# Optimization experiments

Hardware: AMD Instinct MI355X
Metric: run time of the kernel (lower is better)

Reference implementation:

```python
import jax, jax.numpy as jnp
import numpy as np

H = 16          # num_heads
KVH = 4         # num_kv_heads
HD = 128        # head_dim = dim // num_heads
BASE = 10000.0  # rope_base
EPS = 1.1920928955078125e-07  # torch F.rms_norm default eps = finfo(fp32).eps


def rotate_half(x):
    h = x.shape[-1] // 2
    return jnp.concatenate([-x[..., h:], x[..., :h]], axis=-1)


def rms_norm(x):
    return x * jax.lax.rsqrt(jnp.mean(x * x, axis=-1, keepdims=True) + EPS)


def setup_inputs() -> dict:
    key = jax.random.key(0)
    ks = jax.random.split(key, 5)
    D = H * HD
    KVD = KVH * HD
    s = 0.02
    x = jax.random.normal(ks[0], (4, 2048, D), jnp.float32)
    Wq = jax.random.normal(ks[1], (D, D), jnp.float32) * s
    Wk = jax.random.normal(ks[2], (KVD, D), jnp.float32) * s
    Wv = jax.random.normal(ks[3], (KVD, D), jnp.float32) * s
    Wproj = jax.random.normal(ks[4], (D, D), jnp.float32) * s
    q_gain = jnp.full((H,), 1.0, jnp.float32)
    return {"x": x, "Wq": Wq, "Wk": Wk, "Wv": Wv, "Wproj": Wproj, "q_gain": q_gain}


def reference(x, Wq, Wk, Wv, Wproj, q_gain):
    B, T, D = x.shape
    # QKV projections (bias-free), reshape to [B, heads, T, head_dim]
    q = (x @ Wq.T).reshape(B, T, H, HD).transpose(0, 2, 1, 3)
    k = (x @ Wk.T).reshape(B, T, KVH, HD).transpose(0, 2, 1, 3)
    v = (x @ Wv.T).reshape(B, T, KVH, HD).transpose(0, 2, 1, 3)
    # QK RMSNorm (no learned weight)
    q = rms_norm(q)
    k = rms_norm(k)
    # Rotary embedding tables [T, HD]
    t = jnp.arange(T, dtype=jnp.float32)
    inv_freq = 1.0 / (BASE ** (jnp.arange(0, HD, 2, dtype=jnp.float32) / HD))
    freqs = jnp.outer(t, inv_freq)
    emb = jnp.concatenate([freqs, freqs], axis=-1)
    cos, sin = jnp.cos(emb), jnp.sin(emb)
    # RoPE + per-head gain on q
    q = (q * cos + rotate_half(q) * sin) * q_gain[None, :, None, None]
    k = k * cos + rotate_half(k) * sin
    # GQA: repeat_interleave kv heads to match q heads
    groups = H // KVH
    k = jnp.repeat(k, groups, axis=1)
    v = jnp.repeat(v, groups, axis=1)
    # Causal scaled dot-product attention
    scores = jnp.einsum('bhqd,bhkd->bhqk', q, k) / np.float32(np.sqrt(HD))
    mask = jnp.tril(jnp.ones((T, T), dtype=bool))
    scores = jnp.where(mask, scores, -jnp.inf)
    attn = jax.nn.softmax(scores, axis=-1)
    y = jnp.einsum('bhqk,bhkd->bhqd', attn, v)
    y = y.transpose(0, 2, 1, 3).reshape(B, T, D)
    return y @ Wproj.T
```

## Files before the change

### kernel.cpp

```cpp
#include <hip/hip_runtime.h>
#include <math.h>


typedef float f32x4 __attribute__((ext_vector_type(4)));
typedef __bf16 bf16x8 __attribute__((ext_vector_type(8)));
typedef __bf16 bf16x4 __attribute__((ext_vector_type(4)));

__device__ __forceinline__ void load_lds16(const __bf16* g, __bf16* l) {
    __builtin_amdgcn_global_load_lds(
        (const __attribute__((address_space(1))) void*)g,
        (__attribute__((address_space(3))) void*)l, 16, 0, 0);
}

__global__ __launch_bounds__(256) void cvt_f32_bf16(
    const float* __restrict__ src, __bf16* __restrict__ dst, int n)
{
    int i = (blockIdx.x * 256 + threadIdx.x) * 4;
    if (i < n) {
        float4 v = *(const float4*)(src + i);
        bf16x4 o = {(__bf16)v.x, (__bf16)v.y, (__bf16)v.z, (__bf16)v.w};
        *(bf16x4*)(dst + i) = o;
    }
}

template <int NI, typename OutT>
__global__ __launch_bounds__(512, 2) void gemm256(
    const __bf16* __restrict__ A, const __bf16* __restrict__ W,
    OutT* __restrict__ C, int M, int N, int K)
{
    constexpr int BN = 64 * NI;
    const int bn = blockIdx.x, bm = blockIdx.y;
    const int tid = threadIdx.x;
    const int lane = tid & 63;
    const int wave = tid >> 6;
    const int quad = lane >> 4, l16 = lane & 15;
    const int wm2 = wave >> 2;
    const int wn4 = wave & 3;

    __shared__ __bf16 As[2][256 * 64];
    __shared__ __bf16 Bs[2][BN * 64];

    f32x4 acc[8][NI] = {};

    const int sr = tid >> 3;
    const int sc = tid & 7;
    const int scs = sc ^ (sr & 7);

    const __bf16* Ag = A + (size_t)(bm * 256 + sr) * K + scs * 8;
    const __bf16* Wg = W + (size_t)(bn * BN + sr) * K + scs * 8;
    __bf16* Asd = &As[0][0] + sr * 64 + sc * 8;
    __bf16* Bsd = &Bs[0][0] + sr * 64 + sc * 8;

    auto stage = [&](int t, int h) {
        const int k0 = t * 64;
#pragma unroll
        for (int ra = 0; ra < 4; ++ra)
            load_lds16(Ag + (size_t)(ra * 64) * K + k0,
                       Asd + h * 16384 + ra * 4096);
#pragma unroll
        for (int rb = 0; rb < NI; ++rb)
            load_lds16(Wg + (size_t)(rb * 64) * K + k0,
                       Bsd + h * (BN * 64) + rb * 4096);
    };
    auto wait_prev = [&]() {
        if constexpr (NI == 4) asm volatile("s_waitcnt vmcnt(8)" ::: "memory");
        else                   asm volatile("s_waitcnt vmcnt(6)" ::: "memory");
    };

    const int NT = K / 64;

    stage(0, 0);
    stage(1, 1);
    wait_prev();
    asm volatile("" ::: "memory");
    __builtin_amdgcn_s_barrier();
    asm volatile("" ::: "memory");

    for (int t = 0; t < NT; ++t) {
        const int h = t & 1;
        const __bf16* Ab = &As[h][0];
        const __bf16* Bb = &Bs[h][0];

        bf16x8 bfr[NI][2];
#pragma unroll
        for (int ph = 0; ph < 4; ++ph) {
            bf16x8 af[2][2];
#pragma unroll
            for (int j = 0; j < 2; ++j)
#pragma unroll
                for (int ks = 0; ks < 2; ++ks)
                    af[j][ks] = *(const bf16x8*)(
                        Ab + (wm2 * 128 + (ph * 2 + j) * 16 + l16) * 64 +
                        (((ks * 4 + quad) ^ (l16 & 7)) * 8));
            if (ph == 0) {
#pragma unroll
                for (int ni = 0; ni < NI; ++ni)
#pragma unroll
                    for (int ks = 0; ks < 2; ++ks)
                        bfr[ni][ks] = *(const bf16x8*)(
                            Bb + (wn4 * 16 * NI + ni * 16 + l16) * 64 +
                            (((ks * 4 + quad) ^ (l16 & 7)) * 8));
            }
            asm volatile("" ::: "memory");
            __builtin_amdgcn_s_barrier();
            asm volatile("" ::: "memory");
            __builtin_amdgcn_s_setprio(1);
#pragma unroll
            for (int j = 0; j < 2; ++j)
#pragma unroll
                for (int ni = 0; ni < NI; ++ni)
#pragma unroll
                    for (int ks = 0; ks < 2; ++ks)
                        acc[ph * 2 + j][ni] = __builtin_amdgcn_mfma_f32_16x16x32_bf16(
                            af[j][ks], bfr[ni][ks], acc[ph * 2 + j][ni], 0, 0, 0);
            __builtin_amdgcn_s_setprio(0);
            asm volatile("" ::: "memory");
            __builtin_amdgcn_s_barrier();
            asm volatile("" ::: "memory");
        }

        if (t + 2 < NT) {
            stage(t + 2, h);
            wait_prev();
        } else if (t + 1 < NT) {
            asm volatile("s_waitcnt vmcnt(0)" ::: "memory");
        } else {
            break;
        }
        asm volatile("" ::: "memory");
        __builtin_amdgcn_s_barrier();
        asm volatile("" ::: "memory");
    }

#pragma unroll
    for (int mi = 0; mi < 8; ++mi) {
#pragma unroll
        for (int r = 0; r < 4; ++r) {
            int row = bm * 256 + wm2 * 128 + mi * 16 + quad * 4 + r;
            OutT* Cp = C + (size_t)row * N + bn * BN + wn4 * 16 * NI + l16;
#pragma unroll
            for (int ni = 0; ni < NI; ++ni)
                Cp[ni * 16] = (OutT)acc[mi][ni][r];
        }
    }
}

__global__ __launch_bounds__(256) void qk_norm_rope(
    __bf16* __restrict__ q, __bf16* __restrict__ kv,
    const float* __restrict__ q_gain)
{
    const int row = blockIdx.x * 4 + (threadIdx.x >> 6);
    const int lane = threadIdx.x & 63;
    const int BTH = 4 * 2048 * 16;

    __bf16* base;
    int t;
    float gain;
    if (row < BTH) {
        int bt = row >> 4, h = row & 15;
        base = q + (size_t)bt * 2048 + h * 128;
        t = bt & 2047;
        gain = q_gain[h];
    } else {
        int r2 = row - BTH;
        int bt = r2 >> 2, kvh = r2 & 3;
        base = kv + (size_t)bt * 1024 + kvh * 128;
        t = bt & 2047;
        gain = 1.0f;
    }

    float x0 = (float)base[lane];
    float x1 = (float)base[lane + 64];

    float ss = x0 * x0 + x1 * x1;
#pragma unroll
    for (int off = 32; off; off >>= 1) ss += __shfl_xor(ss, off);
    float inv = rsqrtf(ss * (1.0f / 128.0f) + 1.1920928955078125e-07f);
    x0 *= inv; x1 *= inv;

    float freq = exp2f(-(float)lane * 0.20762050593046013f);
    float ang = (float)t * freq;
    float s, c;
    sincosf(ang, &s, &c);
    float o0 = x0 * c - x1 * s;
    float o1 = x1 * c + x0 * s;
    base[lane]      = (__bf16)(o0 * gain);
    base[lane + 64] = (__bf16)(o1 * gain);
}

__global__ __launch_bounds__(256) void transpose_v(
    const __bf16* __restrict__ kv, __bf16* __restrict__ vtout)
{
    __shared__ __bf16 tile[64][65];
    const int b = blockIdx.z;
    const int t0 = blockIdx.x * 64, c0 = blockIdx.y * 64;
    const __bf16* vb = kv + (size_t)b * 2048 * 1024 + 512;
    __bf16* vtb = vtout + (size_t)b * 512 * 2048;
    const int j = threadIdx.x & 63;
    const int r0 = threadIdx.x >> 6;
#pragma unroll
    for (int i = 0; i < 16; ++i) {
        int r = r0 + i * 4;
        tile[r][j] = vb[(size_t)(t0 + r) * 1024 + c0 + j];
    }
    __syncthreads();
#pragma unroll
    for (int i = 0; i < 16; ++i) {
        int r = r0 + i * 4;
        vtb[(size_t)(c0 + r) * 2048 + t0 + j] = tile[j][r];
    }
}

__global__ __launch_bounds__(256, 2) void attn(
    const __bf16* __restrict__ q, const __bf16* __restrict__ kv,
    const __bf16* __restrict__ vt, __bf16* __restrict__ y,
    const float* __restrict__ q_gain)
{
    const int qt = 15 - blockIdx.y;
    const int bh = blockIdx.x;
    const int b = bh >> 4, h = bh & 15, kvh = h >> 2;
    const int tid = threadIdx.x;
    const int wave = tid >> 6, lane = tid & 63;
    const int quad = lane >> 4, l16 = lane & 15;

    __shared__ __bf16 Ks[2][64 * 128];
    __shared__ __bf16 Vts[2][128 * 64];
    __shared__ __bf16 Ps[4 * 16 * 64];

    const int qt0 = qt * 128;
    const int wq = wave * 16;

    bf16x8 qf[2][4];
#pragma unroll
    for (int p = 0; p < 2; ++p) {
        const size_t qrow =
            ((size_t)b * 2048 + qt0 + p * 64 + wq + l16) * 2048 + h * 128;
#pragma unroll
        for (int t = 0; t < 4; ++t)
            qf[p][t] = *(const bf16x8*)(q + qrow + t * 32 + quad * 8);
    }

    f32x4 oacc[2][8] = {};
    float lsum[2][4] = {};

    const float sm_scale = 0.12754635f;
    const float mfix = 11.5f * fabsf(q_gain[h]);

    const size_t kbase = (size_t)b * 2048 * 1024 + kvh * 128;
    const size_t vtbase = (size_t)(b * 4 + kvh) * 128 * 2048;

    const int rowK = lane >> 4, pcK = lane & 15;
    const int rowV = lane >> 3, pcV = lane & 7;

    const int nj = 2 * qt + 2;

    {
#pragma unroll
        for (int r = 0; r < 4; ++r) {
            int rrK = (r * 4 + wave) * 4 + rowK;
            int cK = pcK ^ (rrK & 15);
            load_lds16(kv + kbase + (size_t)rrK * 1024 + cK * 8,
                       &Ks[0][(r * 4 + wave) * 512]);
            int rrV = (r * 4 + wave) * 8 + rowV;
            int cV = pcV ^ (rrV & 7);
            load_lds16(vt + vtbase + (size_t)rrV * 2048 + cV * 8,
                       &Vts[0][(r * 4 + wave) * 512]);
        }
    }

    for (int jt = 0; jt < nj; ++jt) {
        const int cur = jt & 1;

        asm volatile("" ::: "memory");
        __builtin_amdgcn_s_barrier();
        asm volatile("" ::: "memory");

        if (jt + 1 < nj) {
            const int j0n = (jt + 1) * 64;
#pragma unroll
            for (int r = 0; r < 4; ++r) {
                int rrK = (r * 4 + wave) * 4 + rowK;
                int cK = pcK ^ (rrK & 15);
                load_lds16(kv + kbase + (size_t)(j0n + rrK) * 1024 + cK * 8,
                           &Ks[cur ^ 1][(r * 4 + wave) * 512]);
                int rrV = (r * 4 + wave) * 8 + rowV;
                int cV = pcV ^ (rrV & 7);
                load_lds16(vt + vtbase + (size_t)rrV * 2048 + j0n + cV * 8,
                           &Vts[cur ^ 1][(r * 4 + wave) * 512]);
            }
            asm volatile("s_waitcnt vmcnt(8)" ::: "memory");
        } else {
            asm volatile("s_waitcnt vmcnt(0)" ::: "memory");
        }

        asm volatile("" ::: "memory");
        __builtin_amdgcn_s_barrier();
        asm volatile("" ::: "memory");

        const __bf16* Kc = Ks[cur];
        const __bf16* Vc = Vts[cur];

#pragma unroll
        for (int p = 0; p < 2; ++p) {
            const int dlim = 2 * qt + p;
            if (jt > dlim) continue;

            f32x4 sacc[4] = {};
#pragma unroll
            for (int nt = 0; nt < 4; ++nt)
#pragma unroll
                for (int t = 0; t < 4; ++t) {
                    bf16x8 kf = *(const bf16x8*)(
                        Kc + (nt * 16 + l16) * 128 + ((t * 4 + quad) ^ l16) * 8);
                    sacc[nt] = __builtin_amdgcn_mfma_f32_16x16x32_bf16(
                        qf[p][t], kf, sacc[nt], 0, 0, 0);
                }

            if (jt == dlim) {
#pragma unroll
                for (int nt = 0; nt < 4; ++nt) {
                    int kg = nt * 16 + l16;
#pragma unroll
                    for (int r = 0; r < 4; ++r)
                        if (kg > wq + quad * 4 + r) sacc[nt][r] = -3.0e38f;
                }
            }

            float pv4[4][4];
#pragma unroll
            for (int nt = 0; nt < 4; ++nt)
#pragma unroll
                for (int r = 0; r < 4; ++r) {
                    float pv = exp2f((sacc[nt][r] - mfix) * sm_scale);
                    pv4[nt][r] = pv;
                    lsum[p][r] += pv;
                }

            __bf16* Pw = Ps + wave * 1024;
#pragma unroll
            for (int nt = 0; nt < 4; ++nt)
#pragma unroll
                for (int r = 0; r < 4; ++r) {
                    int row = quad * 4 + r;
                    int pc = (nt * 2 + (l16 >> 3)) ^ (row & 7);
                    Pw[row * 64 + pc * 8 + (l16 & 7)] = (__bf16)pv4[nt][r];
                }

#pragma unroll
            for (int kt = 0; kt < 2; ++kt) {
                bf16x8 pf = *(const bf16x8*)(
                    Pw + l16 * 64 + ((kt * 4 + quad) ^ (l16 & 7)) * 8);
#pragma unroll
                for (int vn = 0; vn < 8; ++vn) {
                    bf16x8 vf = *(const bf16x8*)(
                        Vc + (vn * 16 + l16) * 64 + ((kt * 4 + quad) ^ (l16 & 7)) * 8);
                    oacc[p][vn] = __builtin_amdgcn_mfma_f32_16x16x32_bf16(
                        pf, vf, oacc[p][vn], 0, 0, 0);
                }
            }
        }
    }

#pragma unroll
    for (int p = 0; p < 2; ++p) {
#pragma unroll
        for (int r = 0; r < 4; ++r)
#pragma unroll
            for (int off = 8; off; off >>= 1)
                lsum[p][r] += __shfl_xor(lsum[p][r], off);

        const size_t ybase =
            ((size_t)b * 2048 + qt0 + p * 64 + wq) * 2048 + h * 128;
#pragma unroll
        for (int r = 0; r < 4; ++r) {
            float inv = 1.0f / lsum[p][r];
            __bf16* yp = y + ybase + (size_t)(quad * 4 + r) * 2048 + l16;
#pragma unroll
            for (int vn = 0; vn < 8; ++vn)
                yp[vn * 16] = (__bf16)(oacc[p][vn][r] * inv);
        }
    }
}

extern "C" void kernel_launch(void* const* d_in, const int* in_sizes, int n_in,
                              void* d_out, int out_size, void* d_ws, size_t ws_size,
                              hipStream_t stream) {
    const float* x     = (const float*)d_in[0];
    const float* Wq    = (const float*)d_in[1];
    const float* Wk    = (const float*)d_in[2];
    const float* Wv    = (const float*)d_in[3];
    const float* Wproj = (const float*)d_in[4];
    const float* qgain = (const float*)d_in[5];
    float* outp = (float*)d_out;

    __bf16* xb  = (__bf16*)d_ws;
    __bf16* Wqb = xb  + 16777216;
    __bf16* Wkb = Wqb + 4194304;
    __bf16* Wvb = Wkb + 1048576;
    __bf16* Wpb = Wvb + 1048576;
    __bf16* q   = Wpb + 4194304;
    __bf16* kvb = q   + 16777216;
    __bf16* vt  = kvb + 8388608;
    __bf16* y   = q;

    dim3 blk(256);
    cvt_f32_bf16<<<dim3(16777216 / 1024), blk, 0, stream>>>(x, xb, 16777216);
    cvt_f32_bf16<<<dim3(4194304 / 1024), blk, 0, stream>>>(Wq, Wqb, 4194304);
    cvt_f32_bf16<<<dim3(1048576 / 1024), blk, 0, stream>>>(Wk, Wkb, 1048576);
    cvt_f32_bf16<<<dim3(1048576 / 1024), blk, 0, stream>>>(Wv, Wvb, 1048576);
    cvt_f32_bf16<<<dim3(4194304 / 1024), blk, 0, stream>>>(Wproj, Wpb, 4194304);

    gemm256<4, __bf16><<<dim3(8, 32), dim3(512), 0, stream>>>(xb, Wqb, q, 8192, 2048, 2048);
    gemm256<2, __bf16><<<dim3(8, 32), dim3(512), 0, stream>>>(xb, Wkb, kvb, 8192, 1024, 2048);
    qk_norm_rope<<<dim3((4 * 2048 * (16 + 4)) / 4), blk, 0, stream>>>(q, kvb, qgain);
    transpose_v<<<dim3(32, 8, 4), blk, 0, stream>>>(kvb, vt);
    attn<<<dim3(64, 16), blk, 0, stream>>>(q, kvb, vt, y, qgain);
    gemm256<4, float><<<dim3(8, 32), dim3(512), 0, stream>>>(y, Wpb, outp, 8192, 2048, 2048);
}
```

Before: 527.6 us.

## Merge conversion launches and interleave both query halves in attention MFMA loops

The five fp32-to-bf16 conversion launches become one kernel that picks the source array from the flat index. In the attention inner loop, the two 64-row query halves are now processed together: each K and V fragment load feeds two MFMAs, P is staged in two LDS buffers, and MFMA sections run at raised wave priority via s_setprio. This drops the per-half skip, so the second half always computes scores for the extra diagonal tile and relies on masking. It cuts LDS fragment reloads and launch overhead in exchange for more registers and some wasted MFMA work.

Result: faster. 513.1 us (-2.8%).

```diff
diff --git a/kernel.cpp b/kernel.cpp
--- a/kernel.cpp
+++ b/kernel.cpp
@@ -12,15 +12,23 @@
         (__attribute__((address_space(3))) void*)l, 16, 0, 0);
 }
 
-__global__ __launch_bounds__(256) void cvt_f32_bf16(
-    const float* __restrict__ src, __bf16* __restrict__ dst, int n)
+__global__ __launch_bounds__(256) void cvt_all(
+    const float* __restrict__ x,  const float* __restrict__ Wq,
+    const float* __restrict__ Wk, const float* __restrict__ Wv,
+    const float* __restrict__ Wp, __bf16* __restrict__ dst)
 {
-    int i = (blockIdx.x * 256 + threadIdx.x) * 4;
-    if (i < n) {
-        float4 v = *(const float4*)(src + i);
-        bf16x4 o = {(__bf16)v.x, (__bf16)v.y, (__bf16)v.z, (__bf16)v.w};
-        *(bf16x4*)(dst + i) = o;
-    }
+    long long i = ((long long)blockIdx.x * 256 + threadIdx.x) * 4;
+    if (i >= 27262976LL) return;
+    const float* src;
+    long long off;
+    if (i < 16777216LL)      { src = x;  off = i; }
+    else if (i < 20971520LL) { src = Wq; off = i - 16777216LL; }
+    else if (i < 22020096LL) { src = Wk; off = i - 20971520LL; }
+    else if (i < 23068672LL) { src = Wv; off = i - 22020096LL; }
+    else                     { src = Wp; off = i - 23068672LL; }
+    float4 v = *(const float4*)(src + off);
+    bf16x4 o = {(__bf16)v.x, (__bf16)v.y, (__bf16)v.z, (__bf16)v.w};
+    *(bf16x4*)(dst + i) = o;
 }
 
 template <int NI, typename OutT>
@@ -225,7 +233,7 @@
 
     __shared__ __bf16 Ks[2][64 * 128];
     __shared__ __bf16 Vts[2][128 * 64];
-    __shared__ __bf16 Ps[4 * 16 * 64];
+    __shared__ __bf16 Ps[2][4 * 16 * 64];
 
     const int qt0 = qt * 128;
     const int wq = wave * 16;
@@ -300,65 +308,68 @@
         const __bf16* Kc = Ks[cur];
         const __bf16* Vc = Vts[cur];
 
-#pragma unroll
-        for (int p = 0; p < 2; ++p) {
-            const int dlim = 2 * qt + p;
-            if (jt > dlim) continue;
-
-            f32x4 sacc[4] = {};
-#pragma unroll
-            for (int nt = 0; nt < 4; ++nt)
-#pragma unroll
-                for (int t = 0; t < 4; ++t) {
-                    bf16x8 kf = *(const bf16x8*)(
-                        Kc + (nt * 16 + l16) * 128 + ((t * 4 + quad) ^ l16) * 8);
-                    sacc[nt] = __builtin_amdgcn_mfma_f32_16x16x32_bf16(
-                        qf[p][t], kf, sacc[nt], 0, 0, 0);
-                }
-
-            if (jt == dlim) {
+        f32x4 sacc[2][4] = {};
+        __builtin_amdgcn_s_setprio(1);
+#pragma unroll
+        for (int nt = 0; nt < 4; ++nt)
+#pragma unroll
+            for (int t = 0; t < 4; ++t) {
+                bf16x8 kf = *(const bf16x8*)(
+                    Kc + (nt * 16 + l16) * 128 + ((t * 4 + quad) ^ l16) * 8);
+                sacc[0][nt] = __builtin_amdgcn_mfma_f32_16x16x32_bf16(
+                    qf[0][t], kf, sacc[0][nt], 0, 0, 0);
+                sacc[1][nt] = __builtin_amdgcn_mfma_f32_16x16x32_bf16(
+                    qf[1][t], kf, sacc[1][nt], 0, 0, 0);
+            }
+        __builtin_amdgcn_s_setprio(0);
+
+        if (jt >= 2 * qt) {
+            const int dj = (jt - 2 * qt) * 64;
+#pragma unroll
+            for (int p = 0; p < 2; ++p) {
+                const int rel = p * 64 + wq + quad * 4 - dj;
 #pragma unroll
                 for (int nt = 0; nt < 4; ++nt) {
                     int kg = nt * 16 + l16;
 #pragma unroll
                     for (int r = 0; r < 4; ++r)
-                        if (kg > wq + quad * 4 + r) sacc[nt][r] = -3.0e38f;
+                        if (kg > rel + r) sacc[p][nt][r] = -3.0e38f;
                 }
             }
-
-            float pv4[4][4];
+        }
+
+#pragma unroll
+        for (int p = 0; p < 2; ++p) {
+            __bf16* Pw = &Ps[p][0] + wave * 1024;
 #pragma unroll
             for (int nt = 0; nt < 4; ++nt)
 #pragma unroll
                 for (int r = 0; r < 4; ++r) {
-                    float pv = exp2f((sacc[nt][r] - mfix) * sm_scale);
-                    pv4[nt][r] = pv;
+                    float pv = exp2f((sacc[p][nt][r] - mfix) * sm_scale);
                     lsum[p][r] += pv;
-                }
-
-            __bf16* Pw = Ps + wave * 1024;
-#pragma unroll
-            for (int nt = 0; nt < 4; ++nt)
-#pragma unroll
-                for (int r = 0; r < 4; ++r) {
                     int row = quad * 4 + r;
                     int pc = (nt * 2 + (l16 >> 3)) ^ (row & 7);
-                    Pw[row * 64 + pc * 8 + (l16 & 7)] = (__bf16)pv4[nt][r];
+                    Pw[row * 64 + pc * 8 + (l16 & 7)] = (__bf16)pv;
                 }
-
-#pragma unroll
-            for (int kt = 0; kt < 2; ++kt) {
-                bf16x8 pf = *(const bf16x8*)(
-                    Pw + l16 * 64 + ((kt * 4 + quad) ^ (l16 & 7)) * 8);
-#pragma unroll
-                for (int vn = 0; vn < 8; ++vn) {
-                    bf16x8 vf = *(const bf16x8*)(
-                        Vc + (vn * 16 + l16) * 64 + ((kt * 4 + quad) ^ (l16 & 7)) * 8);
-                    oacc[p][vn] = __builtin_amdgcn_mfma_f32_16x16x32_bf16(
-                        pf, vf, oacc[p][vn], 0, 0, 0);
-                }
+        }
+
+        __builtin_amdgcn_s_setprio(1);
+#pragma unroll
+        for (int kt = 0; kt < 2; ++kt) {
+            const int pcc = ((kt * 4 + quad) ^ (l16 & 7)) * 8;
+            bf16x8 pf0 = *(const bf16x8*)(&Ps[0][0] + wave * 1024 + l16 * 64 + pcc);
+            bf16x8 pf1 = *(const bf16x8*)(&Ps[1][0] + wave * 1024 + l16 * 64 + pcc);
+#pragma unroll
+            for (int vn = 0; vn < 8; ++vn) {
+                bf16x8 vf = *(const bf16x8*)(
+                    Vc + (vn * 16 + l16) * 64 + pcc);
+                oacc[0][vn] = __builtin_amdgcn_mfma_f32_16x16x32_bf16(
+                    pf0, vf, oacc[0][vn], 0, 0, 0);
+                oacc[1][vn] = __builtin_amdgcn_mfma_f32_16x16x32_bf16(
+                    pf1, vf, oacc[1][vn], 0, 0, 0);
             }
         }
+        __builtin_amdgcn_s_setprio(0);
     }
 
 #pragma unroll
@@ -404,11 +415,7 @@
     __bf16* y   = q;
 
     dim3 blk(256);
-    cvt_f32_bf16<<<dim3(16777216 / 1024), blk, 0, stream>>>(x, xb, 16777216);
-    cvt_f32_bf16<<<dim3(4194304 / 1024), blk, 0, stream>>>(Wq, Wqb, 4194304);
-    cvt_f32_bf16<<<dim3(1048576 / 1024), blk, 0, stream>>>(Wk, Wkb, 1048576);
-    cvt_f32_bf16<<<dim3(1048576 / 1024), blk, 0, stream>>>(Wv, Wvb, 1048576);
-    cvt_f32_bf16<<<dim3(4194304 / 1024), blk, 0, stream>>>(Wproj, Wpb, 4194304);
+    cvt_all<<<dim3(27262976 / 1024), blk, 0, stream>>>(x, Wq, Wk, Wv, Wproj, xb);
 
     gemm256<4, __bf16><<<dim3(8, 32), dim3(512), 0, stream>>>(xb, Wqb, q, 8192, 2048, 2048);
     gemm256<2, __bf16><<<dim3(8, 32), dim3(512), 0, stream>>>(xb, Wkb, kvb, 8192, 1024, 2048);
```
